# Performance work log

Hardware: AMD Instinct MI355X
Metric: run time of the kernel (lower is better)

Reference implementation:

```python
import jax, jax.numpy as jnp
import numpy as np

P_DIM, L_DIM, D, O = 1100, 1024, 1024, 1024  # protein/label embed dims, latent, mlp width
B, NL = 16, 5000  # num_sequences, num_labels


def setup_inputs() -> dict:
    key = jax.random.key(0)
    ks = jax.random.split(key, 10)
    s = 0.02
    return {
        "sequence_embeddings": jax.random.normal(ks[0], (B, P_DIM), jnp.float32),
        "label_embeddings": jax.random.normal(ks[1], (NL, L_DIM), jnp.float32),
        "Wp": jax.random.normal(ks[2], (D, P_DIM), jnp.float32) * s,  # W_p (no bias)
        "Wl": jax.random.normal(ks[3], (D, L_DIM), jnp.float32) * s,  # W_l (no bias)
        "W1": jax.random.normal(ks[4], (O, 2 * D), jnp.float32) * s,  # Linear(2D -> O)
        "b1": jnp.zeros((O,), jnp.float32),
        "W2": jax.random.normal(ks[5], (O, O), jnp.float32) * s,      # Linear(O -> O)
        "b2": jnp.zeros((O,), jnp.float32),
        "W3": jax.random.normal(ks[6], (1, O), jnp.float32) * s,      # Linear(O -> 1)
        "b3": jnp.zeros((1,), jnp.float32),
    }


def reference(sequence_embeddings, label_embeddings, Wp, Wl, W1, b1, W2, b2, W3, b3):
    # Latent projections
    P_e = sequence_embeddings @ Wp.T           # [B, D]
    L_e = label_embeddings @ Wl.T              # [NL, D]
    # First MLP layer on concat([P_e, L_e]) over the cross join, computed by
    # splitting W1 into its P and L halves and broadcast-summing (same math as
    # cat + Linear, avoids materializing the [B*NL, 2D] concat).
    hp = P_e @ W1[:, :D].T                     # [B, O]
    hl = L_e @ W1[:, D:].T                     # [NL, O]
    h = jax.nn.relu(hp[:, None, :] + hl[None, :, :] + b1)   # [B, NL, O]
    h = jax.nn.relu(h @ W2.T + b2)             # [B, NL, O]
    logits = (h @ W3.T + b3)[..., 0]           # [B, NL]
    return logits
```

## Files before the change

### kernel.cpp

```cpp
#include <hip/hip_runtime.h>
#include <hip/hip_bf16.h>
#include <stdint.h>

typedef __bf16 bf16;
typedef __bf16 bf16x4 __attribute__((ext_vector_type(4)));
typedef __bf16 bf16x8 __attribute__((ext_vector_type(8)));
typedef float floatx4 __attribute__((ext_vector_type(4)));

#define B_SEQ 16
#define NLBL  5000
#define DLAT  1024
#define PDIM  1100
#define NROWS (B_SEQ * NLBL)

__device__ __forceinline__ void gload_lds16(const bf16* g, bf16* l) {
    __builtin_amdgcn_global_load_lds(
        (const __attribute__((address_space(1))) void*)g,
        (__attribute__((address_space(3))) void*)l, 16, 0, 0);
}

__device__ __forceinline__ bf16x8 cvt8(const float* s) {
    floatx4 a = *(const floatx4*)s;
    floatx4 b = *(const floatx4*)(s + 4);
    bf16x8 o;
    o[0] = (bf16)a.x; o[1] = (bf16)a.y; o[2] = (bf16)a.z; o[3] = (bf16)a.w;
    o[4] = (bf16)b.x; o[5] = (bf16)b.y; o[6] = (bf16)b.z; o[7] = (bf16)b.w;
    return o;
}

__device__ __forceinline__ void barx() {
    asm volatile("" ::: "memory");
    __builtin_amdgcn_s_barrier();
    asm volatile("" ::: "memory");
}

#define PSEG_M    256
#define PSEG_LAB  2756
#define PSEG_W2   3268
#define PSEG_PE   3524
#define PSEG_END  3837

__global__ __launch_bounds__(256)
void prep_kernel(const float* __restrict__ label, bf16* __restrict__ label_b,
                 const float* __restrict__ W2, bf16* __restrict__ W2_b,
                 const float* __restrict__ W1, const float* __restrict__ Wl,
                 bf16* __restrict__ M_bf,
                 const float* __restrict__ seq, const float* __restrict__ Wp,
                 float* __restrict__ Pe,
                 float* __restrict__ out, const float* __restrict__ b3) {
    __shared__ bf16 MAs[64 * 72];
    __shared__ bf16 MBs[64 * 72];
    const int blk = blockIdx.x;
    const int t = threadIdx.x;

    if (blk < PSEG_M) {
        const int m0 = (blk >> 4) * 64;
        const int n0g = (blk & 15) * 64;
        const int wave = t >> 6, lane = t & 63;
        const int wm = (wave & 1) * 32, wn = (wave >> 1) * 32;
        const int lm = lane & 15, quad = lane >> 4;
        const int a_r = t >> 2, a_c = (t & 3) * 16;
        const int b_kr = t >> 4, b_l = (t & 15) * 4;
        floatx4 acc[2][2] = {};

        for (int k0 = 0; k0 < 1024; k0 += 64) {
            const float* ap = W1 + (size_t)(m0 + a_r) * 2048 + 1024 + k0 + a_c;
            *(bf16x8*)(MAs + a_r * 72 + a_c) = cvt8(ap);
            *(bf16x8*)(MAs + a_r * 72 + a_c + 8) = cvt8(ap + 8);
#pragma unroll
            for (int ps = 0; ps < 4; ++ps) {
                int kr = b_kr + ps * 16;
                floatx4 v = *(const floatx4*)(Wl + (size_t)(k0 + kr) * 1024 + n0g + b_l);
                MBs[(b_l + 0) * 72 + kr] = (bf16)v.x;
                MBs[(b_l + 1) * 72 + kr] = (bf16)v.y;
                MBs[(b_l + 2) * 72 + kr] = (bf16)v.z;
                MBs[(b_l + 3) * 72 + kr] = (bf16)v.w;
            }
            __syncthreads();
#pragma unroll
            for (int ks = 0; ks < 2; ++ks) {
                bf16x8 af[2], bg[2];
#pragma unroll
                for (int mi = 0; mi < 2; ++mi)
                    af[mi] = *(const bf16x8*)(MAs + (wm + mi * 16 + lm) * 72 + ks * 32 + quad * 8);
#pragma unroll
                for (int ni = 0; ni < 2; ++ni)
                    bg[ni] = *(const bf16x8*)(MBs + (wn + ni * 16 + lm) * 72 + ks * 32 + quad * 8);
#pragma unroll
                for (int mi = 0; mi < 2; ++mi)
#pragma unroll
                    for (int ni = 0; ni < 2; ++ni)
                        acc[mi][ni] = __builtin_amdgcn_mfma_f32_16x16x32_bf16(af[mi], bg[ni], acc[mi][ni], 0, 0, 0);
            }
            __syncthreads();
        }
#pragma unroll
        for (int mi = 0; mi < 2; ++mi)
#pragma unroll
            for (int r = 0; r < 4; ++r)
#pragma unroll
                for (int ni = 0; ni < 2; ++ni)
                    M_bf[(size_t)(m0 + wm + mi * 16 + quad * 4 + r) * 1024 + n0g + wn + ni * 16 + lm] =
                        (bf16)acc[mi][ni][r];
    } else if (blk < PSEG_LAB) {
        int i = (blk - PSEG_M) * 256 + t;
        ((bf16x8*)label_b)[i] = cvt8(label + (size_t)i * 8);
    } else if (blk < PSEG_W2) {
        int i = (blk - PSEG_LAB) * 256 + t;
        ((bf16x8*)W2_b)[i] = cvt8(W2 + (size_t)i * 8);
    } else if (blk < PSEG_PE) {
        int w = (blk - PSEG_W2) * 4 + (t >> 6);
        int l = t & 63;
        floatx4 wv[5];
#pragma unroll
        for (int k = 0; k < 5; ++k) {
            int g = l + 64 * k;
            wv[k] = (g < 275) ? *(const floatx4*)(Wp + (size_t)w * PDIM + g * 4)
                              : floatx4{0.f, 0.f, 0.f, 0.f};
        }
        for (int b = 0; b < B_SEQ; ++b) {
            float acc = 0.f;
#pragma unroll
            for (int k = 0; k < 5; ++k) {
                int g = l + 64 * k;
                if (g < 275) {
                    floatx4 sv = *(const floatx4*)(seq + (size_t)b * PDIM + g * 4);
                    acc += wv[k].x * sv.x + wv[k].y * sv.y + wv[k].z * sv.z + wv[k].w * sv.w;
                }
            }
#pragma unroll
            for (int off = 32; off; off >>= 1) acc += __shfl_xor(acc, off, 64);
            if (l == 0) Pe[b * DLAT + w] = acc;
        }
    } else {
        int i = (blk - PSEG_PE) * 256 + t;
        if (i < NROWS) out[i] = b3[0];
    }
}


__global__ __launch_bounds__(256)
void hpb_kernel(const float* __restrict__ Pe, const float* __restrict__ W1,
                const float* __restrict__ b1, float* __restrict__ hpb) {
    int w = blockIdx.x * 4 + (threadIdx.x >> 6);
    int l = threadIdx.x & 63;
    floatx4 wv[4];
#pragma unroll
    for (int k = 0; k < 4; ++k)
        wv[k] = *(const floatx4*)(W1 + (size_t)w * 2048 + (l + 64 * k) * 4);
    for (int b = 0; b < B_SEQ; ++b) {
        float acc = 0.f;
#pragma unroll
        for (int k = 0; k < 4; ++k) {
            floatx4 pv = *(const floatx4*)(Pe + (size_t)b * DLAT + (l + 64 * k) * 4);
            acc += wv[k].x * pv.x + wv[k].y * pv.y + wv[k].z * pv.z + wv[k].w * pv.w;
        }
#pragma unroll
        for (int off = 32; off; off >>= 1) acc += __shfl_xor(acc, off, 64);
        if (l == 0) hpb[b * DLAT + w] = acc + b1[w];
    }
}


__global__ __launch_bounds__(256)
void hl_h1_kernel(const bf16* __restrict__ A, const bf16* __restrict__ Bt,
                  const float* __restrict__ hpb, bf16* __restrict__ h1) {
    __shared__ __align__(16) char smem[25600];
    bf16* As = (bf16*)smem;
    bf16* Bs = (bf16*)(smem + 8192);
    bf16* Ls = (bf16*)smem;
    float* hpbs = (float*)(smem + 17408);

    const int t = threadIdx.x;
    const int d0 = blockIdx.x * 128;
    const int n0 = blockIdx.y * 64;
    const int wave = t >> 6, lane = t & 63;
    const int wm = (wave & 1) * 32;
    const int wn = (wave >> 1) * 64;
    const int lm = lane & 15, quad = lane >> 4;
    const int sw = lm & 7;
    const int srow = t >> 3;
    const int scg0 = t & 7;
    const int sbase = (t & 192) * 8;

    floatx4 acc[2][4] = {};

    for (int k0 = 0; k0 < 1024; k0 += 64) {
#pragma unroll
        for (int p = 0; p < 2; ++p) {
            int row = p * 32 + srow;
            int cg = scg0 ^ (row & 7);
            int grow = n0 + row; if (grow >= NLBL) grow = NLBL - 1;
            gload_lds16(A + (size_t)grow * 1024 + k0 + cg * 8, As + p * 2048 + sbase);
        }
#pragma unroll
        for (int p = 0; p < 4; ++p) {
            int row = p * 32 + srow;
            int cg = scg0 ^ (row & 7);
            gload_lds16(Bt + (size_t)(d0 + row) * 1024 + k0 + cg * 8, Bs + p * 2048 + sbase);
        }
        __syncthreads();
#pragma unroll
        for (int k = 0; k < 64; k += 32) {
            bf16x8 af[2], bg[4];
            int ko = (((k >> 3) + quad) ^ sw) * 8;
#pragma unroll
            for (int mi = 0; mi < 2; ++mi)
                af[mi] = *(const bf16x8*)(As + (wm + mi * 16 + lm) * 64 + ko);
#pragma unroll
            for (int ni = 0; ni < 4; ++ni)
                bg[ni] = *(const bf16x8*)(Bs + (wn + ni * 16 + lm) * 64 + ko);
#pragma unroll
            for (int mi = 0; mi < 2; ++mi)
#pragma unroll
                for (int ni = 0; ni < 4; ++ni)
                    acc[mi][ni] = __builtin_amdgcn_mfma_f32_16x16x32_bf16(af[mi], bg[ni], acc[mi][ni], 0, 0, 0);
        }
        __syncthreads();
    }

#pragma unroll
    for (int mi = 0; mi < 2; ++mi)
#pragma unroll
        for (int r = 0; r < 4; ++r)
#pragma unroll
            for (int ni = 0; ni < 4; ++ni)
                Ls[(wm + mi * 16 + quad * 4 + r) * 136 + wn + ni * 16 + lm] =
                    (bf16)acc[mi][ni][r];
    {
        int dl = (t & 31) * 4;
        int b = t >> 5;
        *(floatx4*)(hpbs + b * 128 + dl) =
            *(const floatx4*)(hpb + (size_t)b * DLAT + d0 + dl);
        *(floatx4*)(hpbs + (b + 8) * 128 + dl) =
            *(const floatx4*)(hpb + (size_t)(b + 8) * DLAT + d0 + dl);
    }
    __syncthreads();

    const int g = t & 15;
    const int r0 = t >> 4;
    bf16x8 hlv[4];
#pragma unroll
    for (int p = 0; p < 4; ++p)
        hlv[p] = *(const bf16x8*)(Ls + (p * 16 + r0) * 136 + g * 8);

    for (int b = 0; b < B_SEQ; ++b) {
        floatx4 h0 = *(const floatx4*)(hpbs + b * 128 + g * 8);
        floatx4 h4 = *(const floatx4*)(hpbs + b * 128 + g * 8 + 4);
        size_t rowbase = (size_t)b * NLBL * 1024;
#pragma unroll
        for (int p = 0; p < 4; ++p) {
            int n = n0 + p * 16 + r0;
            if (n >= NLBL) continue;
            bf16x8 o;
            o[0] = (bf16)fmaxf((float)hlv[p][0] + h0.x, 0.f);
            o[1] = (bf16)fmaxf((float)hlv[p][1] + h0.y, 0.f);
            o[2] = (bf16)fmaxf((float)hlv[p][2] + h0.z, 0.f);
            o[3] = (bf16)fmaxf((float)hlv[p][3] + h0.w, 0.f);
            o[4] = (bf16)fmaxf((float)hlv[p][4] + h4.x, 0.f);
            o[5] = (bf16)fmaxf((float)hlv[p][5] + h4.y, 0.f);
            o[6] = (bf16)fmaxf((float)hlv[p][6] + h4.z, 0.f);
            o[7] = (bf16)fmaxf((float)hlv[p][7] + h4.w, 0.f);
            *(bf16x8*)(h1 + rowbase + (size_t)n * 1024 + d0 + g * 8) = o;
        }
    }
}


__device__ __forceinline__ void stage_A256(const bf16* __restrict__ src, bf16* dst,
                                           int m0, int kc, int t) {
#pragma unroll
    for (int i = 0; i < 4; ++i) {
        int s = t + i * 512;
        int row = s >> 3;
        int cg = (s & 7) ^ (row & 7);
        int grow = m0 + row;
        if (grow >= NROWS) grow = NROWS - 1;
        gload_lds16(src + (size_t)grow * 1024 + kc + cg * 8, dst + s * 8);
    }
}

__device__ __forceinline__ void stage_B256(const bf16* __restrict__ src, bf16* dst,
                                           int n0, int kc, int t) {
#pragma unroll
    for (int i = 0; i < 4; ++i) {
        int s = t + i * 512;
        int row = s >> 3;
        int cg = (s & 7) ^ (row & 7);
        gload_lds16(src + (size_t)(n0 + row) * 1024 + kc + cg * 8, dst + s * 8);
    }
}

__global__ __launch_bounds__(512, 2)
void gemm_h2(const bf16* __restrict__ h1, const bf16* __restrict__ W2b,
             const float* __restrict__ b2, const float* __restrict__ W3,
             float* __restrict__ out) {
    __shared__ bf16 As[32768];
    __shared__ bf16 Bs[32768];
    const int t = threadIdx.x;

    int orig = blockIdx.x;
    int xcd = orig & 7, idx = orig >> 3;
    int wg = (xcd < 4 ? xcd * 157 : 628 + (xcd - 4) * 156) + idx;
    const int mt = wg >> 2, nt = wg & 3;
    const int m0 = mt * 256, n0 = nt * 256;

    const int wave = t >> 6, lane = t & 63;
    const int wr = wave >> 2, wc = wave & 3;
    const int wrow = wr * 128, wcol = wc * 64;
    const int lm = lane & 15, quad = lane >> 4;
    const int swz = lm & 7;

    floatx4 acc[8][4] = {};

    stage_A256(h1, As, m0, 0, t);
    stage_B256(W2b, Bs, n0, 0, t);
    asm volatile("s_waitcnt vmcnt(0)" ::: "memory");
    barx();

    for (int kt = 0; kt < 16; ++kt) {
        const int db = kt & 1;
        const bf16* Ad = As + db * 16384;
        const bf16* Bd = Bs + db * 16384;
        bf16* An = As + (db ^ 1) * 16384;
        bf16* Bn = Bs + (db ^ 1) * 16384;
        const bool pf = (kt < 15);
        const int kc = (kt + 1) * 64;

        bf16x8 a[4][2], blo[2][2], bhi[2][2];

#pragma unroll
        for (int mi = 0; mi < 4; ++mi) {
            const bf16* rp = Ad + (wrow + mi * 16 + lm) * 64;
            a[mi][0] = *(const bf16x8*)(rp + ((quad ^ swz) << 3));
            a[mi][1] = *(const bf16x8*)(rp + (((4 + quad) ^ swz) << 3));
        }
#pragma unroll
        for (int ni = 0; ni < 2; ++ni) {
            const bf16* rp = Bd + (wcol + ni * 16 + lm) * 64;
            blo[ni][0] = *(const bf16x8*)(rp + ((quad ^ swz) << 3));
            blo[ni][1] = *(const bf16x8*)(rp + (((4 + quad) ^ swz) << 3));
        }
        if (pf) stage_A256(h1, An, m0, kc, t);
        barx();
        __builtin_amdgcn_s_setprio(1);
#pragma unroll
        for (int ks = 0; ks < 2; ++ks)
#pragma unroll
            for (int mi = 0; mi < 4; ++mi)
#pragma unroll
                for (int ni = 0; ni < 2; ++ni)
                    acc[mi][ni] = __builtin_amdgcn_mfma_f32_16x16x32_bf16(a[mi][ks], blo[ni][ks], acc[mi][ni], 0, 0, 0);
        __builtin_amdgcn_s_setprio(0);
        barx();

#pragma unroll
        for (int ni = 0; ni < 2; ++ni) {
            const bf16* rp = Bd + (wcol + 32 + ni * 16 + lm) * 64;
            bhi[ni][0] = *(const bf16x8*)(rp + ((quad ^ swz) << 3));
            bhi[ni][1] = *(const bf16x8*)(rp + (((4 + quad) ^ swz) << 3));
        }
        if (pf) stage_B256(W2b, Bn, n0, kc, t);
        barx();
        __builtin_amdgcn_s_setprio(1);
#pragma unroll
        for (int ks = 0; ks < 2; ++ks)
#pragma unroll
            for (int mi = 0; mi < 4; ++mi)
#pragma unroll
                for (int ni = 0; ni < 2; ++ni)
                    acc[mi][2 + ni] = __builtin_amdgcn_mfma_f32_16x16x32_bf16(a[mi][ks], bhi[ni][ks], acc[mi][2 + ni], 0, 0, 0);
        __builtin_amdgcn_s_setprio(0);
        barx();

#pragma unroll
        for (int mi = 0; mi < 4; ++mi) {
            const bf16* rp = Ad + (wrow + 64 + mi * 16 + lm) * 64;
            a[mi][0] = *(const bf16x8*)(rp + ((quad ^ swz) << 3));
            a[mi][1] = *(const bf16x8*)(rp + (((4 + quad) ^ swz) << 3));
        }
        barx();
        __builtin_amdgcn_s_setprio(1);
#pragma unroll
        for (int ks = 0; ks < 2; ++ks)
#pragma unroll
            for (int mi = 0; mi < 4; ++mi)
#pragma unroll
                for (int ni = 0; ni < 2; ++ni)
                    acc[4 + mi][2 + ni] = __builtin_amdgcn_mfma_f32_16x16x32_bf16(a[mi][ks], bhi[ni][ks], acc[4 + mi][2 + ni], 0, 0, 0);
        __builtin_amdgcn_s_setprio(0);
        barx();

        __builtin_amdgcn_s_setprio(1);
#pragma unroll
        for (int ks = 0; ks < 2; ++ks)
#pragma unroll
            for (int mi = 0; mi < 4; ++mi)
#pragma unroll
                for (int ni = 0; ni < 2; ++ni)
                    acc[4 + mi][ni] = __builtin_amdgcn_mfma_f32_16x16x32_bf16(a[mi][ks], blo[ni][ks], acc[4 + mi][ni], 0, 0, 0);
        __builtin_amdgcn_s_setprio(0);
        asm volatile("s_waitcnt vmcnt(0)" ::: "memory");
        barx();
    }

    float w3v[4], b2v[4];
#pragma unroll
    for (int ni = 0; ni < 4; ++ni) {
        int col = n0 + wcol + ni * 16 + lm;
        w3v[ni] = W3[col];
        b2v[ni] = b2[col];
    }
#pragma unroll
    for (int mi = 0; mi < 8; ++mi) {
#pragma unroll
        for (int r = 0; r < 4; ++r) {
            float sacc = 0.f;
#pragma unroll
            for (int ni = 0; ni < 4; ++ni)
                sacc += fmaxf(acc[mi][ni][r] + b2v[ni], 0.f) * w3v[ni];
            sacc += __shfl_xor(sacc, 1, 64);
            sacc += __shfl_xor(sacc, 2, 64);
            sacc += __shfl_xor(sacc, 4, 64);
            sacc += __shfl_xor(sacc, 8, 64);
            int row = m0 + wrow + mi * 16 + quad * 4 + r;
            if (lm == 0 && row < NROWS)
                atomicAdd(out + row, sacc);
        }
    }
}


extern "C" void kernel_launch(void* const* d_in, const int* in_sizes, int n_in,
                              void* d_out, int out_size, void* d_ws, size_t ws_size,
                              hipStream_t stream) {
    const float* seq   = (const float*)d_in[0];
    const float* label = (const float*)d_in[1];
    const float* Wp    = (const float*)d_in[2];
    const float* Wl    = (const float*)d_in[3];
    const float* W1    = (const float*)d_in[4];
    const float* b1    = (const float*)d_in[5];
    const float* W2    = (const float*)d_in[6];
    const float* b2    = (const float*)d_in[7];
    const float* W3    = (const float*)d_in[8];
    const float* b3    = (const float*)d_in[9];
    float* out = (float*)d_out;
    (void)n_in; (void)in_sizes; (void)out_size; (void)ws_size;

    size_t off = 0;
    auto alloc = [&](size_t bytes) {
        void* p = (char*)d_ws + off;
        off += (bytes + 255) & ~(size_t)255;
        return p;
    };
    bf16* label_b = (bf16*)alloc((size_t)NLBL * 1024 * 2);
    bf16* W2_b    = (bf16*)alloc((size_t)1024 * 1024 * 2);
    bf16* M_bf    = (bf16*)alloc((size_t)1024 * 1024 * 2);
    float* Pe     = (float*)alloc((size_t)B_SEQ * 1024 * 4);
    float* hpb    = (float*)alloc((size_t)B_SEQ * 1024 * 4);
    bf16* h1      = (bf16*)alloc((size_t)NROWS * 1024 * 2);

    prep_kernel<<<PSEG_END, 256, 0, stream>>>(label, label_b, W2, W2_b, W1, Wl,
                                              M_bf, seq, Wp, Pe, out, b3);
    hpb_kernel<<<256, 256, 0, stream>>>(Pe, W1, b1, hpb);
    hl_h1_kernel<<<dim3(8, 79), 256, 0, stream>>>(label_b, M_bf, hpb, h1);
    gemm_h2<<<1252, 512, 0, stream>>>(h1, W2_b, b2, W3, out);
}
```

Measured before the change: 326.8 us.

## Stage GEMM tiles in half-tile chunks with two-deep prefetch and partial waits

Splits the LDS staging of the 256x64 A and B tiles into 128-row halves and interleaves the loads for k-step kt+1 and kt+2 between the four MFMA quadrant phases. The wait becomes vmcnt(6), so loads stay in flight across iterations instead of draining every step. The warp-to-tile mapping also changes, so each wave now covers interleaved 64-row and 32-col slices from both halves. This aims to hide global-load latency behind MFMA work, at the cost of tighter ordering rules on when each half-buffer may be overwritten.

Result: slower. 342.0 us (+4.7%).

```diff
diff --git a/kernel.cpp b/kernel.cpp
--- a/kernel.cpp
+++ b/kernel.cpp
@@ -267,27 +267,27 @@
 }
 
 
-__device__ __forceinline__ void stage_A256(const bf16* __restrict__ src, bf16* dst,
-                                           int m0, int kc, int t) {
-#pragma unroll
-    for (int i = 0; i < 4; ++i) {
+__device__ __forceinline__ void stage_halfA(const bf16* __restrict__ src, bf16* dst,
+                                            int m0, int roff, int kc, int t) {
+#pragma unroll
+    for (int i = 0; i < 2; ++i) {
         int s = t + i * 512;
-        int row = s >> 3;
+        int row = roff + (s >> 3);
         int cg = (s & 7) ^ (row & 7);
         int grow = m0 + row;
         if (grow >= NROWS) grow = NROWS - 1;
-        gload_lds16(src + (size_t)grow * 1024 + kc + cg * 8, dst + s * 8);
-    }
-}
-
-__device__ __forceinline__ void stage_B256(const bf16* __restrict__ src, bf16* dst,
-                                           int n0, int kc, int t) {
-#pragma unroll
-    for (int i = 0; i < 4; ++i) {
+        gload_lds16(src + (size_t)grow * 1024 + kc + cg * 8, dst + row * 64 + (s & 7) * 8);
+    }
+}
+
+__device__ __forceinline__ void stage_halfB(const bf16* __restrict__ src, bf16* dst,
+                                            int n0, int roff, int kc, int t) {
+#pragma unroll
+    for (int i = 0; i < 2; ++i) {
         int s = t + i * 512;
-        int row = s >> 3;
+        int row = roff + (s >> 3);
         int cg = (s & 7) ^ (row & 7);
-        gload_lds16(src + (size_t)(n0 + row) * 1024 + kc + cg * 8, dst + s * 8);
+        gload_lds16(src + (size_t)(n0 + row) * 1024 + kc + cg * 8, dst + row * 64 + (s & 7) * 8);
     }
 }
 
@@ -307,41 +307,48 @@
 
     const int wave = t >> 6, lane = t & 63;
     const int wr = wave >> 2, wc = wave & 3;
-    const int wrow = wr * 128, wcol = wc * 64;
     const int lm = lane & 15, quad = lane >> 4;
     const int swz = lm & 7;
+    const int sl0 = (quad ^ swz) << 3;
+    const int sl1 = ((4 + quad) ^ swz) << 3;
 
     floatx4 acc[8][4] = {};
-
-    stage_A256(h1, As, m0, 0, t);
-    stage_B256(W2b, Bs, n0, 0, t);
-    asm volatile("s_waitcnt vmcnt(0)" ::: "memory");
+    bf16x8 a[4][2], b0f[2][2], b1f[2][2];
+
+    stage_halfA(h1, As, m0, 0, 0, t);
+    stage_halfB(W2b, Bs, n0, 0, 0, t);
+    stage_halfB(W2b, Bs, n0, 128, 0, t);
+    stage_halfA(h1, As, m0, 128, 0, t);
+    stage_halfA(h1, As + 16384, m0, 0, 64, t);
+    stage_halfB(W2b, Bs + 16384, n0, 0, 64, t);
+    stage_halfB(W2b, Bs + 16384, n0, 128, 64, t);
+    asm volatile("s_waitcnt vmcnt(6)" ::: "memory");
     barx();
 
     for (int kt = 0; kt < 16; ++kt) {
         const int db = kt & 1;
         const bf16* Ad = As + db * 16384;
         const bf16* Bd = Bs + db * 16384;
-        bf16* An = As + (db ^ 1) * 16384;
-        bf16* Bn = Bs + (db ^ 1) * 16384;
-        const bool pf = (kt < 15);
-        const int kc = (kt + 1) * 64;
-
-        bf16x8 a[4][2], blo[2][2], bhi[2][2];
+        bf16* Aoth = As + (db ^ 1) * 16384;
+        bf16* Acur = As + db * 16384;
+        bf16* Bcur = Bs + db * 16384;
+        const int kc1 = (kt + 1) * 64;
+        const int kc2 = (kt + 2) * 64;
+        const bool p1 = (kt < 15), p2 = (kt < 14);
 
 #pragma unroll
         for (int mi = 0; mi < 4; ++mi) {
-            const bf16* rp = Ad + (wrow + mi * 16 + lm) * 64;
-            a[mi][0] = *(const bf16x8*)(rp + ((quad ^ swz) << 3));
-            a[mi][1] = *(const bf16x8*)(rp + (((4 + quad) ^ swz) << 3));
+            const bf16* rp = Ad + (wr * 64 + mi * 16 + lm) * 64;
+            a[mi][0] = *(const bf16x8*)(rp + sl0);
+            a[mi][1] = *(const bf16x8*)(rp + sl1);
         }
 #pragma unroll
         for (int ni = 0; ni < 2; ++ni) {
-            const bf16* rp = Bd + (wcol + ni * 16 + lm) * 64;
-            blo[ni][0] = *(const bf16x8*)(rp + ((quad ^ swz) << 3));
-            blo[ni][1] = *(const bf16x8*)(rp + (((4 + quad) ^ swz) << 3));
-        }
-        if (pf) stage_A256(h1, An, m0, kc, t);
+            const bf16* rp = Bd + (wc * 32 + ni * 16 + lm) * 64;
+            b0f[ni][0] = *(const bf16x8*)(rp + sl0);
+            b0f[ni][1] = *(const bf16x8*)(rp + sl1);
+        }
+        if (p1) stage_halfA(h1, Aoth, m0, 128, kc1, t);
         barx();
         __builtin_amdgcn_s_setprio(1);
 #pragma unroll
@@ -350,17 +357,17 @@
             for (int mi = 0; mi < 4; ++mi)
 #pragma unroll
                 for (int ni = 0; ni < 2; ++ni)
-                    acc[mi][ni] = __builtin_amdgcn_mfma_f32_16x16x32_bf16(a[mi][ks], blo[ni][ks], acc[mi][ni], 0, 0, 0);
+                    acc[mi][ni] = __builtin_amdgcn_mfma_f32_16x16x32_bf16(a[mi][ks], b0f[ni][ks], acc[mi][ni], 0, 0, 0);
         __builtin_amdgcn_s_setprio(0);
         barx();
 
 #pragma unroll
         for (int ni = 0; ni < 2; ++ni) {
-            const bf16* rp = Bd + (wcol + 32 + ni * 16 + lm) * 64;
-            bhi[ni][0] = *(const bf16x8*)(rp + ((quad ^ swz) << 3));
-            bhi[ni][1] = *(const bf16x8*)(rp + (((4 + quad) ^ swz) << 3));
-        }
-        if (pf) stage_B256(W2b, Bn, n0, kc, t);
+            const bf16* rp = Bd + (128 + wc * 32 + ni * 16 + lm) * 64;
+            b1f[ni][0] = *(const bf16x8*)(rp + sl0);
+            b1f[ni][1] = *(const bf16x8*)(rp + sl1);
+        }
+        if (p2) stage_halfA(h1, Acur, m0, 0, kc2, t);
         barx();
         __builtin_amdgcn_s_setprio(1);
 #pragma unroll
@@ -369,16 +376,17 @@
             for (int mi = 0; mi < 4; ++mi)
 #pragma unroll
                 for (int ni = 0; ni < 2; ++ni)
-                    acc[mi][2 + ni] = __builtin_amdgcn_mfma_f32_16x16x32_bf16(a[mi][ks], bhi[ni][ks], acc[mi][2 + ni], 0, 0, 0);
+                    acc[mi][2 + ni] = __builtin_amdgcn_mfma_f32_16x16x32_bf16(a[mi][ks], b1f[ni][ks], acc[mi][2 + ni], 0, 0, 0);
         __builtin_amdgcn_s_setprio(0);
         barx();
 
 #pragma unroll
         for (int mi = 0; mi < 4; ++mi) {
-            const bf16* rp = Ad + (wrow + 64 + mi * 16 + lm) * 64;
-            a[mi][0] = *(const bf16x8*)(rp + ((quad ^ swz) << 3));
-            a[mi][1] = *(const bf16x8*)(rp + (((4 + quad) ^ swz) << 3));
-        }
+            const bf16* rp = Ad + (128 + wr * 64 + mi * 16 + lm) * 64;
+            a[mi][0] = *(const bf16x8*)(rp + sl0);
+            a[mi][1] = *(const bf16x8*)(rp + sl1);
+        }
+        if (p2) stage_halfB(W2b, Bcur, n0, 0, kc2, t);
         barx();
         __builtin_amdgcn_s_setprio(1);
 #pragma unroll
@@ -387,10 +395,11 @@
             for (int mi = 0; mi < 4; ++mi)
 #pragma unroll
                 for (int ni = 0; ni < 2; ++ni)
-                    acc[4 + mi][2 + ni] = __builtin_amdgcn_mfma_f32_16x16x32_bf16(a[mi][ks], bhi[ni][ks], acc[4 + mi][2 + ni], 0, 0, 0);
+                    acc[4 + mi][ni] = __builtin_amdgcn_mfma_f32_16x16x32_bf16(a[mi][ks], b0f[ni][ks], acc[4 + mi][ni], 0, 0, 0);
         __builtin_amdgcn_s_setprio(0);
         barx();
 
+        if (p2) stage_halfB(W2b, Bcur, n0, 128, kc2, t);
         __builtin_amdgcn_s_setprio(1);
 #pragma unroll
         for (int ks = 0; ks < 2; ++ks)
@@ -398,16 +407,21 @@
             for (int mi = 0; mi < 4; ++mi)
 #pragma unroll
                 for (int ni = 0; ni < 2; ++ni)
-                    acc[4 + mi][ni] = __builtin_amdgcn_mfma_f32_16x16x32_bf16(a[mi][ks], blo[ni][ks], acc[4 + mi][ni], 0, 0, 0);
+                    acc[4 + mi][2 + ni] = __builtin_amdgcn_mfma_f32_16x16x32_bf16(a[mi][ks], b1f[ni][ks], acc[4 + mi][2 + ni], 0, 0, 0);
         __builtin_amdgcn_s_setprio(0);
-        asm volatile("s_waitcnt vmcnt(0)" ::: "memory");
-        barx();
+        if (kt <= 13) {
+            asm volatile("s_waitcnt vmcnt(6)" ::: "memory");
+            barx();
+        } else if (kt == 14) {
+            asm volatile("s_waitcnt vmcnt(0)" ::: "memory");
+            barx();
+        }
     }
 
     float w3v[4], b2v[4];
 #pragma unroll
     for (int ni = 0; ni < 4; ++ni) {
-        int col = n0 + wcol + ni * 16 + lm;
+        int col = n0 + ((ni & 2) ? 128 : 0) + wc * 32 + (ni & 1) * 16 + lm;
         w3v[ni] = W3[col];
         b2v[ni] = b2[col];
     }
@@ -423,7 +437,7 @@
             sacc += __shfl_xor(sacc, 2, 64);
             sacc += __shfl_xor(sacc, 4, 64);
             sacc += __shfl_xor(sacc, 8, 64);
-            int row = m0 + wrow + mi * 16 + quad * 4 + r;
+            int row = m0 + ((mi >= 4) ? 128 : 0) + wr * 64 + (mi & 3) * 16 + quad * 4 + r;
             if (lm == 0 && row < NROWS)
                 atomicAdd(out + row, sacc);
         }
```
